# Kernel tuning notes

Measured on AMD Instinct MI355X. Metric: run time of the kernel, lower is better.

The kernel has to match this reference:

```python
import jax, jax.numpy as jnp
import numpy as np

N, L, H, D = 2, 4096, 12, 64
HD = H * D

def setup_inputs() -> dict:
    key = jax.random.key(0)
    ks = jax.random.split(key, 5)
    s = 1.0 / np.sqrt(HD)  # keep projections well-scaled
    return {
        "x": jax.random.normal(ks[0], (N, L, HD), dtype=jnp.float32),
        "Wq": jax.random.normal(ks[1], (HD, HD), dtype=jnp.float32) * s,
        "bq": jnp.zeros((HD,), dtype=jnp.float32),
        "Wk": jax.random.normal(ks[2], (HD, HD), dtype=jnp.float32) * s,
        "bk": jnp.zeros((HD,), dtype=jnp.float32),
        "Wv": jax.random.normal(ks[3], (HD, HD), dtype=jnp.float32) * s,
        "bv": jnp.zeros((HD,), dtype=jnp.float32),
        "Wo": jax.random.normal(ks[4], (HD, HD), dtype=jnp.float32) * s,
        "bo": jnp.zeros((HD,), dtype=jnp.float32),
        "train": 0,
    }

def reference(x, Wq, bq, Wk, bk, Wv, bv, Wo, bo, train):
    n, l, hd = x.shape
    h, d = H, D
    # QKV projections (hk.Linear: x @ W + b), reshape to (n, l, h, d)
    q = (x @ Wq + bq).reshape(n, l, h, d)
    k = (x @ Wk + bk).reshape(n, l, h, d)
    v = (x @ Wv + bv).reshape(n, l, h, d)
    # scores: (n, q, k, h), scaled by sqrt(key_size)
    qkt = jnp.einsum('nqhd,nkhd->nqkh', q, k) / jnp.sqrt(jnp.float32(d))
    attn = jax.nn.softmax(qkt, axis=2)
    # eval mode: dropout_rate is 0.0, so dropout is identity
    o = jnp.einsum('nqkh,nkhd->nqhd', attn, v).reshape(n, l, hd)
    return o @ Wo + bo
```

## Files before the change

kernel.cpp:

```cpp
#include <hip/hip_runtime.h>

#define NN 2
#define LL 4096
#define HH 12
#define DD 64
#define HD_ 768
#define M_TOT (NN * LL)
#define KVSTRIDE 262144

typedef __bf16 bf16_t;
typedef _Float16 f16_t;
typedef __bf16 bf16x8 __attribute__((ext_vector_type(8)));
typedef __bf16 bf16x4 __attribute__((ext_vector_type(4)));
typedef _Float16 f16x2 __attribute__((ext_vector_type(2)));
typedef _Float16 f16x4 __attribute__((ext_vector_type(4)));
typedef _Float16 f16x8 __attribute__((ext_vector_type(8)));
typedef float floatx4 __attribute__((ext_vector_type(4)));
typedef float floatx16 __attribute__((ext_vector_type(16)));

#define QSCALE 0.1803368801111f

__device__ __forceinline__ void async_load16(const void* g, void* l) {
    __builtin_amdgcn_global_load_lds(
        (const __attribute__((address_space(1))) unsigned int*)(g),
        (__attribute__((address_space(3))) unsigned int*)(l),
        16, 0, 0);
}

__device__ __forceinline__ f16x2 pkrtz(float a, float b) {
    return __builtin_bit_cast(f16x2, __builtin_amdgcn_cvt_pkrtz(a, b));
}

struct PrepArgs { const float* x; bf16_t* xb; const float* W[4]; bf16_t* Wt[4]; };
#define CVT_BLOCKS 6144
__global__ __launch_bounds__(256) void prep_kernel(PrepArgs a) {
    __shared__ bf16_t T[64 * 65];
    const int bid = blockIdx.x;
    const int tid = threadIdx.x;
    if (bid < CVT_BLOCKS) {
        const int i = bid * 256 + tid;
        const float4 v = ((const float4*)a.x)[i];
        bf16_t* d = a.xb + (size_t)i * 4;
        d[0] = (bf16_t)v.x; d[1] = (bf16_t)v.y; d[2] = (bf16_t)v.z; d[3] = (bf16_t)v.w;
        return;
    }
    int r = bid - CVT_BLOCKS;
    const int z = r / 144; r -= z * 144;
    const int k0 = (r / 12) * 64, n0 = (r % 12) * 64;
    {
        const int k = tid >> 2;
        const int nc = (tid & 3) * 16;
        const float* src = a.W[z] + (size_t)(k0 + k) * HD_ + n0 + nc;
        for (int i = 0; i < 4; ++i) {
            float4 v = *(const float4*)(src + i * 4);
            T[(nc + i * 4 + 0) * 65 + k] = (bf16_t)v.x;
            T[(nc + i * 4 + 1) * 65 + k] = (bf16_t)v.y;
            T[(nc + i * 4 + 2) * 65 + k] = (bf16_t)v.z;
            T[(nc + i * 4 + 3) * 65 + k] = (bf16_t)v.w;
        }
    }
    __syncthreads();
    {
        const int n = tid >> 2;
        const int kc = (tid & 3) * 16;
        bf16_t* dst = a.Wt[z] + (size_t)(n0 + n) * HD_ + k0 + kc;
        bf16x8 v0, v1;
        for (int j = 0; j < 8; ++j) { v0[j] = T[n * 65 + kc + j]; v1[j] = T[n * 65 + kc + 8 + j]; }
        *(bf16x8*)dst = v0;
        *(bf16x8*)(dst + 8) = v1;
    }
}

__device__ __forceinline__ void gemm_tile128(
    const bf16_t* __restrict__ A, const bf16_t* __restrict__ Bt,
    bf16_t* As, bf16_t* Bs, int m0, int n0, floatx4 (&acc)[4][4])
{
    const int tid  = threadIdx.x;
    const int w    = tid >> 6, lane = tid & 63;
    const int quad = lane >> 4, l16 = lane & 15;
    const int wm = w >> 1, wn = w & 1;
    const int rsub = lane >> 3;
    const int csub = (lane & 7) * 8;

    const bf16_t* aBase = A + (size_t)(m0 + w * 32 + rsub) * HD_ + csub;
    const bf16_t* bBase = Bt + (size_t)(n0 + w * 32 + rsub) * HD_ + csub;

    for (int kt = 0; kt < HD_; kt += 64) {
        __syncthreads();
        for (int i = 0; i < 4; ++i) {
            const int ar = w * 32 + i * 8;
            async_load16(aBase + (size_t)i * 8 * HD_ + kt, As + ar * 64 + lane * 8);
            async_load16(bBase + (size_t)i * 8 * HD_ + kt, Bs + ar * 64 + lane * 8);
        }
        __syncthreads();
        for (int ks = 0; ks < 2; ++ks) {
            bf16x8 af[4], bf[4];
            for (int mi = 0; mi < 4; ++mi)
                af[mi] = *(const bf16x8*)&As[(wm * 64 + mi * 16 + l16) * 64 + ks * 32 + quad * 8];
            for (int ni = 0; ni < 4; ++ni)
                bf[ni] = *(const bf16x8*)&Bs[(wn * 64 + ni * 16 + l16) * 64 + ks * 32 + quad * 8];
            for (int mi = 0; mi < 4; ++mi)
                for (int ni = 0; ni < 4; ++ni)
                    acc[mi][ni] = __builtin_amdgcn_mfma_f32_16x16x32_bf16(
                        af[mi], bf[ni], acc[mi][ni], 0, 0, 0);
        }
    }
}

struct QKVArgs {
    const bf16_t* Bt[3];
    const float* bias[3];
    void* out[3];
};
__global__ __launch_bounds__(256) void gemm_qkv_kernel(const bf16_t* __restrict__ A, QKVArgs p)
{
    __shared__ __align__(16) bf16_t S[2 * 128 * 64];
    const int z = blockIdx.z;
    const int m0 = blockIdx.y * 128, n0 = blockIdx.x * 128;

    floatx4 acc[4][4] = {};
    gemm_tile128(A, p.Bt[z], S, S + 8192, m0, n0, acc);

    const int tid  = threadIdx.x;
    const int lane = tid & 63;
    const int quad = lane >> 4, l16 = lane & 15;
    const int w    = tid >> 6;
    const int wm = w >> 1, wn = w & 1;
    const float scale = (z == 0) ? QSCALE : 1.0f;
    const float* bias = p.bias[z];

    __syncthreads();
    for (int ni = 0; ni < 4; ++ni) {
        const int dl = ni * 16 + l16;
        const float bv = bias[n0 + wn * 64 + dl];
        for (int mi = 0; mi < 4; ++mi) {
            for (int r = 0; r < 4; ++r) {
                const int ll = wm * 64 + mi * 16 + quad * 4 + r;
                const float val = (acc[mi][ni][r] + bv) * scale;
                int off;
                if (z == 0)
                    off = ll * 64 + dl;
                else if (z == 1)
                    off = ((ll >> 5) * 4 + (dl >> 4)) * 512
                        + ((ll & 31) + 32 * ((dl >> 3) & 1)) * 8 + (dl & 7);
                else
                    off = (((ll >> 6) * 2 + (dl >> 5)) * 4 + ((ll >> 4) & 3)) * 512
                        + ((dl & 31) + 32 * ((ll >> 2) & 1)) * 8
                        + ((ll & 3) + 4 * ((ll >> 3) & 1));
                if (z == 2) ((f16_t*)S)[wn * 8192 + off] = (f16_t)val;
                else        S[wn * 8192 + off] = (bf16_t)val;
            }
        }
    }
    __syncthreads();

    const int ht = tid >> 7, idx = tid & 127;
    const int nn = m0 >> 12, l0 = m0 & 4095;
    const int h = (n0 >> 6) + ht;
    char* dstBase;
    if (z == 0)
        dstBase = (char*)p.out[0] + (((size_t)(nn * HH + h) * LL + l0) * 64) * 2;
    else if (z == 1)
        dstBase = (char*)p.out[1] + ((size_t)(nn * HH + h) * KVSTRIDE + (size_t)(l0 >> 5) * 2048) * 2;
    else
        dstBase = (char*)p.out[2] + ((size_t)(nn * HH + h) * KVSTRIDE + (size_t)(l0 >> 6) * 4096) * 2;
    const bf16_t* srcB = S + ht * 8192;
    for (int c = 0; c < 8; ++c) {
        const int cc = (c + idx) & 7;
        *(bf16x8*)(dstBase + (idx * 64 + cc * 8) * 2) = *(const bf16x8*)(srcB + idx * 64 + cc * 8);
    }
}

__global__ __launch_bounds__(256) void gemm_o_kernel(
    const bf16_t* __restrict__ A, const bf16_t* __restrict__ Bt,
    const float* __restrict__ bias, float* __restrict__ Cout)
{
    __shared__ __align__(16) bf16_t As[128 * 64];
    __shared__ __align__(16) bf16_t Bs[64 * 64];
    const int m0 = blockIdx.y * 128, n0 = blockIdx.x * 64;

    const int tid  = threadIdx.x;
    const int w    = tid >> 6, lane = tid & 63;
    const int quad = lane >> 4, l16 = lane & 15;
    const int rsub = lane >> 3;
    const int csub = (lane & 7) * 8;

    const bf16_t* aBase = A + (size_t)(m0 + w * 32 + rsub) * HD_ + csub;
    const bf16_t* bBase = Bt + (size_t)(n0 + w * 16 + rsub) * HD_ + csub;

    floatx4 acc[2][4] = {};

    for (int kt = 0; kt < HD_; kt += 64) {
        __syncthreads();
        #pragma unroll
        for (int i = 0; i < 4; ++i)
            async_load16(aBase + (size_t)i * 8 * HD_ + kt, As + (w * 32 + i * 8) * 64 + lane * 8);
        #pragma unroll
        for (int i = 0; i < 2; ++i)
            async_load16(bBase + (size_t)i * 8 * HD_ + kt, Bs + (w * 16 + i * 8) * 64 + lane * 8);
        __syncthreads();
        #pragma unroll
        for (int ks = 0; ks < 2; ++ks) {
            bf16x8 af[2], bf[4];
            #pragma unroll
            for (int mi = 0; mi < 2; ++mi)
                af[mi] = *(const bf16x8*)&As[(w * 32 + mi * 16 + l16) * 64 + ks * 32 + quad * 8];
            #pragma unroll
            for (int ni = 0; ni < 4; ++ni)
                bf[ni] = *(const bf16x8*)&Bs[(ni * 16 + l16) * 64 + ks * 32 + quad * 8];
            #pragma unroll
            for (int mi = 0; mi < 2; ++mi)
                #pragma unroll
                for (int ni = 0; ni < 4; ++ni)
                    acc[mi][ni] = __builtin_amdgcn_mfma_f32_16x16x32_bf16(
                        af[mi], bf[ni], acc[mi][ni], 0, 0, 0);
        }
    }

    #pragma unroll
    for (int ni = 0; ni < 4; ++ni) {
        const int col = n0 + ni * 16 + l16;
        const float bv = bias[col];
        #pragma unroll
        for (int mi = 0; mi < 2; ++mi)
            #pragma unroll
            for (int r = 0; r < 4; ++r) {
                const int row = m0 + w * 32 + mi * 16 + quad * 4 + r;
                Cout[(size_t)row * HD_ + col] = acc[mi][ni][r] + bv;
            }
    }
}

__global__ __launch_bounds__(256, 3) void attn_kernel(
    const bf16_t* __restrict__ qg, const bf16_t* __restrict__ kf,
    const f16_t* __restrict__ vf, bf16_t* __restrict__ og)
{
    __shared__ union {
        struct {
            bf16_t Ks[2][4096];
            f16_t  Vs[4][4096];
        } s;
        bf16_t OT[128 * 72];
    } u;

    const int tid = threadIdx.x;
    const int w = tid >> 6, lane = tid & 63;
    const int l32 = lane & 31, hi = lane >> 5;

    const int lb = blockIdx.y * gridDim.x + blockIdx.x;
    const int idx = (lb & 7) * 96 + (lb >> 3);
    const int nh = idx >> 5;
    const int qt0 = (idx & 31) * 128;
    const int nIdx = nh / HH, hIdx = nh % HH;

    bf16x8 qfrag[4];
    {
        const bf16_t* qp = qg + ((size_t)nh * LL + qt0 + w * 32 + l32) * DD + hi * 8;
        for (int s = 0; s < 4; ++s) qfrag[s] = *(const bf16x8*)(qp + s * 16);
    }

    const bf16_t* ksrc = kf + (size_t)nh * KVSTRIDE + (2 * w) * 512 + lane * 8;
    const f16_t*  vsrc = vf + (size_t)nh * KVSTRIDE + (2 * w) * 512 + lane * 8;
    const int soff0 = (2 * w) * 512 + lane * 8;
    const int soff1 = (2 * w + 1) * 512 + lane * 8;

    floatx16 oacc[2] = {};
    float rs = 0.f;
    floatx16 sA0, sA1, sB0, sB1;

#define STAGE_K(kb) { async_load16(ksrc, &u.s.Ks[kb][soff0]);                 \
                      async_load16(ksrc + 512, &u.s.Ks[kb][soff1]);           \
                      ksrc += 4096; }
#define STAGE_V(vb) { async_load16(vsrc, &u.s.Vs[vb][soff0]);                 \
                      async_load16(vsrc + 512, &u.s.Vs[vb][soff1]);           \
                      vsrc += 4096; }

#define SSTEP(SD0, SD1, kr)                                                   \
    {                                                                         \
        SD0 = (floatx16){}; SD1 = (floatx16){};                               \
        _Pragma("unroll")                                                     \
        for (int s = 0; s < 4; ++s) {                                         \
            bf16x8 a0 = *(const bf16x8*)&u.s.Ks[kr][s * 512 + lane * 8];      \
            SD0 = __builtin_amdgcn_mfma_f32_32x32x16_bf16(a0, qfrag[s], SD0, 0, 0, 0); \
            bf16x8 a1 = *(const bf16x8*)&u.s.Ks[kr][(4 + s) * 512 + lane * 8]; \
            SD1 = __builtin_amdgcn_mfma_f32_32x32x16_bf16(a1, qfrag[s], SD1, 0, 0, 0); \
        }                                                                     \
    }

#define PHALF(SC, vp, kvb)                                                    \
    _Pragma("unroll")                                                         \
    for (int sub = 0; sub < 2; ++sub) {                                       \
        float p[8];                                                           \
        _Pragma("unroll")                                                     \
        for (int i = 0; i < 8; ++i)                                           \
            p[i] = __builtin_amdgcn_exp2f(SC[sub * 8 + i]);                   \
        rs += ((p[0] + p[1]) + (p[2] + p[3])) + ((p[4] + p[5]) + (p[6] + p[7])); \
        f16x2 ab = pkrtz(p[0], p[1]), cd = pkrtz(p[2], p[3]);                 \
        f16x2 ef = pkrtz(p[4], p[5]), gh = pkrtz(p[6], p[7]);                 \
        f16x4 lo4 = __builtin_shufflevector(ab, cd, 0, 1, 2, 3);              \
        f16x4 hi4 = __builtin_shufflevector(ef, gh, 0, 1, 2, 3);              \
        f16x8 pf = __builtin_shufflevector(lo4, hi4, 0, 1, 2, 3, 4, 5, 6, 7); \
        const int kstep = (kvb) * 2 + sub;                                    \
        _Pragma("unroll")                                                     \
        for (int db = 0; db < 2; ++db) {                                      \
            f16x8 av = *(const f16x8*)&u.s.Vs[vp][(db * 4 + kstep) * 512 + lane * 8]; \
            oacc[db] = __builtin_amdgcn_mfma_f32_32x32x16_f16(av, pf, oacc[db], 0, 0, 0); \
        }                                                                     \
    }

#define STEP(doDMA, kw, vw, doS, kr, SD0, SD1, SP0, SP1, vp)                  \
    __syncthreads();                                                          \
    if (doDMA) { STAGE_K(kw); STAGE_V(vw); }                                  \
    __builtin_amdgcn_s_setprio(1);                                            \
    if (doS) SSTEP(SD0, SD1, kr);                                             \
    PHALF(SP0, vp, 0)                                                         \
    PHALF(SP1, vp, 1)                                                         \
    __builtin_amdgcn_s_setprio(0);

    STAGE_K(0) STAGE_V(0) STAGE_K(1) STAGE_V(1)
    __syncthreads();
    SSTEP(sA0, sA1, 0);

    for (int t = 0; t < 60; t += 4) {
        STEP(1, 0, 2, 1, 1, sB0, sB1, sA0, sA1, 0)
        STEP(1, 1, 3, 1, 0, sA0, sA1, sB0, sB1, 1)
        STEP(1, 0, 0, 1, 1, sB0, sB1, sA0, sA1, 2)
        STEP(1, 1, 1, 1, 0, sA0, sA1, sB0, sB1, 3)
    }
    STEP(1, 0, 2, 1, 1, sB0, sB1, sA0, sA1, 0)
    STEP(1, 1, 3, 1, 0, sA0, sA1, sB0, sB1, 1)
    STEP(0, 0, 0, 1, 1, sB0, sB1, sA0, sA1, 2)
    STEP(0, 0, 0, 0, 0, sA0, sA1, sB0, sB1, 3)

#undef STEP
#undef PHALF
#undef SSTEP
#undef STAGE_K
#undef STAGE_V

    rs += __shfl_xor(rs, 32);
    const float rinv = __builtin_amdgcn_rcpf(rs);

    __syncthreads();
    for (int db = 0; db < 2; ++db)
        for (int g = 0; g < 4; ++g) {
            bf16x4 o4;
            for (int r = 0; r < 4; ++r)
                o4[r] = (bf16_t)(oacc[db][g * 4 + r] * rinv);
            *(bf16x4*)&u.OT[(w * 32 + l32) * 72 + db * 32 + hi * 4 + g * 8] = o4;
        }
    __syncthreads();

    const int q = tid >> 1, hf = tid & 1;
    const bf16_t* src = &u.OT[q * 72 + hf * 32];
    bf16x8 r0 = *(const bf16x8*)(src + 0);
    bf16x8 r1 = *(const bf16x8*)(src + 8);
    bf16x8 r2 = *(const bf16x8*)(src + 16);
    bf16x8 r3 = *(const bf16x8*)(src + 24);
    bf16_t* dst = og + ((size_t)nIdx * LL + qt0 + q) * HD_ + hIdx * 64 + hf * 32;
    *(bf16x8*)(dst + 0)  = r0;
    *(bf16x8*)(dst + 8)  = r1;
    *(bf16x8*)(dst + 16) = r2;
    *(bf16x8*)(dst + 24) = r3;
}

extern "C" void kernel_launch(void* const* d_in, const int* in_sizes, int n_in,
                              void* d_out, int out_size, void* d_ws, size_t ws_size,
                              hipStream_t stream) {
    const float* x  = (const float*)d_in[0];
    const float* Wq = (const float*)d_in[1];
    const float* bq = (const float*)d_in[2];
    const float* Wk = (const float*)d_in[3];
    const float* bk = (const float*)d_in[4];
    const float* Wv = (const float*)d_in[5];
    const float* bv = (const float*)d_in[6];
    const float* Wo = (const float*)d_in[7];
    const float* bo = (const float*)d_in[8];

    char* ws = (char*)d_ws;
    const size_t xbytes = (size_t)M_TOT * HD_ * 2;
    const size_t wbytes = (size_t)HD_ * HD_ * 2;

    bf16_t* xb  = (bf16_t*)ws; ws += xbytes;
    bf16_t* wqt = (bf16_t*)ws; ws += wbytes;
    bf16_t* wkt = (bf16_t*)ws; ws += wbytes;
    bf16_t* wvt = (bf16_t*)ws; ws += wbytes;
    bf16_t* wot = (bf16_t*)ws; ws += wbytes;
    bf16_t* qb  = (bf16_t*)ws; ws += xbytes;
    bf16_t* kfb = (bf16_t*)ws; ws += xbytes;
    f16_t*  vfb = (f16_t*)ws;  ws += xbytes;
    bf16_t* ob  = (bf16_t*)ws; ws += xbytes;

    PrepArgs pa;
    pa.x = x; pa.xb = xb;
    pa.W[0] = Wq; pa.W[1] = Wk; pa.W[2] = Wv; pa.W[3] = Wo;
    pa.Wt[0] = wqt; pa.Wt[1] = wkt; pa.Wt[2] = wvt; pa.Wt[3] = wot;
    prep_kernel<<<CVT_BLOCKS + 576, 256, 0, stream>>>(pa);

    QKVArgs qa;
    qa.Bt[0] = wqt; qa.Bt[1] = wkt; qa.Bt[2] = wvt;
    qa.bias[0] = bq; qa.bias[1] = bk; qa.bias[2] = bv;
    qa.out[0] = qb; qa.out[1] = kfb; qa.out[2] = vfb;
    gemm_qkv_kernel<<<dim3(HD_ / 128, M_TOT / 128, 3), 256, 0, stream>>>(xb, qa);

    attn_kernel<<<dim3(LL / 128, NN * HH), 256, 0, stream>>>(qb, kfb, vfb, ob);

    gemm_o_kernel<<<dim3(HD_ / 64, M_TOT / 128), 256, 0, stream>>>(ob, wot, bo, (float*)d_out);
}
```

Baseline: 302.7 us.

## Enlarge output GEMM tile to 128x128 and double-buffer LDS loads

The output-projection GEMM now computes a 128x128 tile per block instead of 128x64. Each wave owns a 64x64 sub-tile, which raises MFMA work per LDS fragment load. The A and B stages are double-buffered, so the async global-to-LDS loads for the next K step are issued before the current step is computed, and the loop needs one barrier per iteration instead of two. The grid halves to 384 blocks on a many-CU GPU, which lowers parallelism and may hurt wave occupancy because of more accumulators and twice the LDS.

```diff
diff --git a/kernel.cpp b/kernel.cpp
--- a/kernel.cpp
+++ b/kernel.cpp
@@ -175,57 +175,65 @@
     const bf16_t* __restrict__ A, const bf16_t* __restrict__ Bt,
     const float* __restrict__ bias, float* __restrict__ Cout)
 {
-    __shared__ __align__(16) bf16_t As[128 * 64];
-    __shared__ __align__(16) bf16_t Bs[64 * 64];
-    const int m0 = blockIdx.y * 128, n0 = blockIdx.x * 64;
+    __shared__ __align__(16) bf16_t As[2][128 * 64];
+    __shared__ __align__(16) bf16_t Bs[2][128 * 64];
+    const int m0 = blockIdx.y * 128, n0 = blockIdx.x * 128;
 
     const int tid  = threadIdx.x;
     const int w    = tid >> 6, lane = tid & 63;
     const int quad = lane >> 4, l16 = lane & 15;
+    const int wm = w >> 1, wn = w & 1;
     const int rsub = lane >> 3;
     const int csub = (lane & 7) * 8;
 
     const bf16_t* aBase = A + (size_t)(m0 + w * 32 + rsub) * HD_ + csub;
-    const bf16_t* bBase = Bt + (size_t)(n0 + w * 16 + rsub) * HD_ + csub;
-
-    floatx4 acc[2][4] = {};
-
-    for (int kt = 0; kt < HD_; kt += 64) {
+    const bf16_t* bBase = Bt + (size_t)(n0 + w * 32 + rsub) * HD_ + csub;
+
+    floatx4 acc[4][4] = {};
+
+#define OSTAGE(buf, kt)                                                       \
+    _Pragma("unroll")                                                         \
+    for (int i = 0; i < 4; ++i) {                                             \
+        const int ar = w * 32 + i * 8;                                        \
+        async_load16(aBase + (size_t)i * 8 * HD_ + (kt), &As[buf][ar * 64 + lane * 8]); \
+        async_load16(bBase + (size_t)i * 8 * HD_ + (kt), &Bs[buf][ar * 64 + lane * 8]); \
+    }
+
+    OSTAGE(0, 0)
+
+    int cur = 0;
+    for (int kt = 0; kt < HD_; kt += 64, cur ^= 1) {
         __syncthreads();
-        #pragma unroll
-        for (int i = 0; i < 4; ++i)
-            async_load16(aBase + (size_t)i * 8 * HD_ + kt, As + (w * 32 + i * 8) * 64 + lane * 8);
-        #pragma unroll
-        for (int i = 0; i < 2; ++i)
-            async_load16(bBase + (size_t)i * 8 * HD_ + kt, Bs + (w * 16 + i * 8) * 64 + lane * 8);
-        __syncthreads();
+        if (kt + 64 < HD_) OSTAGE(cur ^ 1, kt + 64)
+
         #pragma unroll
         for (int ks = 0; ks < 2; ++ks) {
-            bf16x8 af[2], bf[4];
+            bf16x8 af[4], bf[4];
             #pragma unroll
-            for (int mi = 0; mi < 2; ++mi)
-                af[mi] = *(const bf16x8*)&As[(w * 32 + mi * 16 + l16) * 64 + ks * 32 + quad * 8];
+            for (int mi = 0; mi < 4; ++mi)
+                af[mi] = *(const bf16x8*)&As[cur][(wm * 64 + mi * 16 + l16) * 64 + ks * 32 + quad * 8];
             #pragma unroll
             for (int ni = 0; ni < 4; ++ni)
-                bf[ni] = *(const bf16x8*)&Bs[(ni * 16 + l16) * 64 + ks * 32 + quad * 8];
+                bf[ni] = *(const bf16x8*)&Bs[cur][(wn * 64 + ni * 16 + l16) * 64 + ks * 32 + quad * 8];
             #pragma unroll
-            for (int mi = 0; mi < 2; ++mi)
+            for (int mi = 0; mi < 4; ++mi)
                 #pragma unroll
                 for (int ni = 0; ni < 4; ++ni)
                     acc[mi][ni] = __builtin_amdgcn_mfma_f32_16x16x32_bf16(
                         af[mi], bf[ni], acc[mi][ni], 0, 0, 0);
         }
     }
+#undef OSTAGE
 
     #pragma unroll
     for (int ni = 0; ni < 4; ++ni) {
-        const int col = n0 + ni * 16 + l16;
+        const int col = n0 + wn * 64 + ni * 16 + l16;
         const float bv = bias[col];
         #pragma unroll
-        for (int mi = 0; mi < 2; ++mi)
+        for (int mi = 0; mi < 4; ++mi)
             #pragma unroll
             for (int r = 0; r < 4; ++r) {
-                const int row = m0 + w * 32 + mi * 16 + quad * 4 + r;
+                const int row = m0 + wm * 64 + mi * 16 + quad * 4 + r;
                 Cout[(size_t)row * HD_ + col] = acc[mi][ni][r] + bv;
             }
     }
@@ -405,5 +413,5 @@
 
     attn_kernel<<<dim3(LL / 128, NN * HH), 256, 0, stream>>>(qb, kfb, vfb, ob);
 
-    gemm_o_kernel<<<dim3(HD_ / 64, M_TOT / 128), 256, 0, stream>>>(ob, wot, bo, (float*)d_out);
-}
+    gemm_o_kernel<<<dim3(HD_ / 128, M_TOT / 128), 256, 0, stream>>>(ob, wot, bo, (float*)d_out);
+}
```

After: 315.0 us. 1.04x slower.
